# Optimization experiments

Hardware: AMD Instinct MI355X
Metric: run time of the kernel (lower is better)

Reference implementation:

```python
import jax, jax.numpy as jnp
import numpy as np

N_EMBD = 64
BLOCK = 8
HEADS = 4
HS = N_EMBD // HEADS  # 16
EPS = 1e-5


def layernorm(x, g, b):
    mu = jnp.mean(x, axis=-1, keepdims=True)
    var = jnp.var(x, axis=-1, keepdims=True)
    return (x - mu) * jax.lax.rsqrt(var + EPS) * g + b


def setup_inputs() -> dict:
    key = jax.random.key(0)
    ks = jax.random.split(key, 12)
    B = 65536
    s = 0.02
    return {
        "x": jax.random.normal(ks[0], (B, BLOCK, N_EMBD), dtype=jnp.float32),
        # per-head Q/K/V projections stacked: [H, C, hs]
        "Wq": jax.random.normal(ks[1], (HEADS, N_EMBD, HS), dtype=jnp.float32) * s,
        "Wk": jax.random.normal(ks[2], (HEADS, N_EMBD, HS), dtype=jnp.float32) * s,
        "Wv": jax.random.normal(ks[3], (HEADS, N_EMBD, HS), dtype=jnp.float32) * s,
        "Wp": jax.random.normal(ks[4], (N_EMBD, N_EMBD), dtype=jnp.float32) * s,
        "bp": jnp.zeros((N_EMBD,), dtype=jnp.float32),
        "W1": jax.random.normal(ks[5], (N_EMBD, 4 * N_EMBD), dtype=jnp.float32) * s,
        "b1": jnp.zeros((4 * N_EMBD,), dtype=jnp.float32),
        "W2": jax.random.normal(ks[6], (4 * N_EMBD, N_EMBD), dtype=jnp.float32) * s,
        "b2": jnp.zeros((N_EMBD,), dtype=jnp.float32),
        "g1": jnp.ones((N_EMBD,), dtype=jnp.float32),
        "beta1": jnp.zeros((N_EMBD,), dtype=jnp.float32),
        "g2": jnp.ones((N_EMBD,), dtype=jnp.float32),
        "beta2": jnp.zeros((N_EMBD,), dtype=jnp.float32),
    }


def reference(x, Wq, Wk, Wv, Wp, bp, W1, b1, W2, b2, g1, beta1, g2, beta2):
    B, T, C = x.shape
    # --- pre-LN self-attention ---
    h = layernorm(x, g1, beta1)
    q = jnp.einsum('btc,hcd->bhtd', h, Wq)
    k = jnp.einsum('btc,hcd->bhtd', h, Wk)
    v = jnp.einsum('btc,hcd->bhtd', h, Wv)
    # NOTE: original scales by n_embd**-0.5 (C of the input), not head_size
    wei = jnp.einsum('bhtd,bhsd->bhts', q, k) * (C ** -0.5)
    tril = jnp.tril(jnp.ones((T, T), dtype=bool))
    wei = jnp.where(tril, wei, -jnp.inf)
    wei = jax.nn.softmax(wei, axis=-1)  # dropout off (eval mode)
    attn = jnp.einsum('bhts,bhsd->bhtd', wei, v)
    attn = attn.transpose(0, 2, 1, 3).reshape(B, T, C)  # concat heads
    sa = attn @ Wp + bp
    x = x + sa
    # --- pre-LN MLP ---
    h2 = layernorm(x, g2, beta2)
    ff = jax.nn.relu(h2 @ W1 + b1) @ W2 + b2
    return x + ff
```

## Files before the change

### kernel.cpp

```cpp
#include <hip/hip_runtime.h>
#include <hip/hip_bf16.h>
#include <stdint.h>

typedef __attribute__((ext_vector_type(8))) short bf16x8;
typedef __attribute__((ext_vector_type(4))) float f32x4;


static __device__ __forceinline__ unsigned short f2bf(float f) {
    union { __hip_bfloat16 h; unsigned short u; } cv;
    cv.h = __float2bfloat16(f);
    return cv.u;
}
static __device__ __forceinline__ unsigned int f2bf2(float a, float b) {
    return (unsigned int)f2bf(a) | ((unsigned int)f2bf(b) << 16);
}
static __device__ __forceinline__ bf16x8 mk8(uint2 a, uint2 b) {
    union { uint4 u; bf16x8 v; } c;
    c.u = make_uint4(a.x, a.y, b.x, b.y);
    return c.v;
}
static __device__ __forceinline__ uint2 packbf(f32x4 a) {
    return make_uint2(f2bf2(a[0], a[1]), f2bf2(a[2], a[3]));
}
static __device__ __forceinline__ uint2 lnq(f32x4 x, float mu, float inv, f32x4 g, f32x4 b) {
    return make_uint2(f2bf2((x[0]-mu)*inv*g[0]+b[0], (x[1]-mu)*inv*g[1]+b[1]),
                      f2bf2((x[2]-mu)*inv*g[2]+b[2], (x[3]-mu)*inv*g[3]+b[3]));
}
static __device__ __forceinline__ uint2 relupack0(f32x4 a) {
    return make_uint2(f2bf2(fmaxf(a[0],0.f), fmaxf(a[1],0.f)),
                      f2bf2(fmaxf(a[2],0.f), fmaxf(a[3],0.f)));
}

#define MFMA(A,B,C) __builtin_amdgcn_mfma_f32_16x16x32_bf16((A),(B),(C),0,0,0)
#define SB() __builtin_amdgcn_sched_barrier(0)

static __device__ __forceinline__ uint2 attn_tail(f32x4 sa, uint2 vw, int fr, int fg) {
    const f32x4 zf = {0.f,0.f,0.f,0.f};
    const uint2 z2 = make_uint2(0u,0u);
    int tk0 = 4*fg, frq = fr & 7;
    bool v8 = ((fr ^ tk0) & 8) == 0;
    float p0 = (v8 && (((tk0+0)&7) <= frq)) ? __expf(sa[0]*0.125f) : 0.f;
    float p1 = (v8 && (((tk0+1)&7) <= frq)) ? __expf(sa[1]*0.125f) : 0.f;
    float p2 = (v8 && (((tk0+2)&7) <= frq)) ? __expf(sa[2]*0.125f) : 0.f;
    float p3 = (v8 && (((tk0+3)&7) <= frq)) ? __expf(sa[3]*0.125f) : 0.f;
    float rsum = p0 + p1 + p2 + p3;
    rsum += __shfl_xor(rsum, 16, 64);
    rsum += __shfl_xor(rsum, 32, 64);
    float pinv = __builtin_amdgcn_rcpf(rsum);
    uint2 pb = make_uint2(f2bf2(p0,p1), f2bf2(p2,p3));
    f32x4 oa = MFMA(mk8(vw, z2), mk8(pb, z2), zf);
    return make_uint2(f2bf2(oa[0]*pinv, oa[1]*pinv), f2bf2(oa[2]*pinv, oa[3]*pinv));
}

static __device__ __forceinline__ void attn_head2(
    bf16x8 wq0, bf16x8 wq1, bf16x8 wk0, bf16x8 wk1, bf16x8 wv0, bf16x8 wv1,
    bf16x8 hA0, bf16x8 hA1, bf16x8 hB0, bf16x8 hB1, int fr, int fg,
    uint2& oA, uint2& oB)
{
    const f32x4 zf = {0.f,0.f,0.f,0.f};
    const uint2 z2 = make_uint2(0u,0u);
    {
        f32x4 qa = MFMA(wq0, hA0, zf); qa = MFMA(wq1, hA1, qa);
        f32x4 ka = MFMA(wk0, hA0, zf); ka = MFMA(wk1, hA1, ka);
        f32x4 va = MFMA(hA0, wv0, zf); va = MFMA(hA1, wv1, va);
        uint2 qw = packbf(qa), kw = packbf(ka), vw = packbf(va);
        f32x4 sa = MFMA(mk8(kw, z2), mk8(qw, z2), zf);
        oA = attn_tail(sa, vw, fr, fg);
    }
    {
        f32x4 qa = MFMA(wq0, hB0, zf); qa = MFMA(wq1, hB1, qa);
        f32x4 ka = MFMA(wk0, hB0, zf); ka = MFMA(wk1, hB1, ka);
        f32x4 va = MFMA(hB0, wv0, zf); va = MFMA(hB1, wv1, va);
        uint2 qw = packbf(qa), kw = packbf(ka), vw = packbf(va);
        f32x4 sa = MFMA(mk8(kw, z2), mk8(qw, z2), zf);
        oB = attn_tail(sa, vw, fr, fg);
    }
}

__global__ __launch_bounds__(512, 1)
void fused_block(const float* __restrict__ xg,
                 const float* __restrict__ Wq, const float* __restrict__ Wk,
                 const float* __restrict__ Wv, const float* __restrict__ Wp,
                 const float* __restrict__ bp, const float* __restrict__ W1,
                 const float* __restrict__ b1, const float* __restrict__ W2,
                 const float* __restrict__ b2, const float* __restrict__ g1,
                 const float* __restrict__ be1, const float* __restrict__ g2,
                 const float* __restrict__ be2, float* __restrict__ out,
                 int nPairsTotal)
{
    __shared__ __align__(16) unsigned char LDS[100864];

    const int tid  = threadIdx.x;
    const int lane = tid & 63;
    const int wid  = tid >> 6;
    const int fr   = lane & 15;
    const int fg   = lane >> 4;

    {
        unsigned short* lw = (unsigned short*)LDS;
        #pragma unroll 1
        for (int e = tid; e < 49152; e += 512) {
            int j = e & 7, ln = (e >> 3) & 63, f = e >> 9;
            int fr_ = ln & 15, fg_ = ln >> 4;
            int u = j >> 2, r_ = j & 3;
            float src;
            if (f < 24) {
                int sel = f >> 3, hd = (f >> 1) & 3, m = f & 1;
                int c = 16*(2*m + u) + 4*fg_ + r_;
                const float* W = (sel == 0) ? Wq : ((sel == 1) ? Wk : Wv);
                src = W[hd*1024 + c*16 + fr_];
            } else if (f < 32) {
                int t = f - 24, nt = t >> 1, m = t & 1;
                int d = 16*(2*m + u) + 4*fg_ + r_;
                src = Wp[d*64 + 16*nt + fr_];
            } else if (f < 64) {
                int t = f - 32, tt = t >> 1, m = t & 1;
                int c = 16*(2*m + u) + 4*fg_ + r_;
                src = W1[c*256 + 16*tt + fr_];
            } else {
                int t = f - 64, nt = t >> 3, m = t & 7;
                int n1 = 16*(2*m + u) + 4*fg_ + r_;
                src = W2[n1*64 + 16*nt + fr_];
            }
            lw[e] = f2bf(src);
        }
    }
    #pragma unroll 1
    for (int t = tid; t < 640; t += 512) {
        float v;
        if      (t < 64)  v = g1[t];
        else if (t < 128) v = be1[t - 64];
        else if (t < 192) v = g2[t - 128];
        else if (t < 256) v = be2[t - 192];
        else if (t < 320) v = bp[t - 256];
        else if (t < 384) v = b2[t - 320];
        else              v = b1[t - 384];
        ((float*)(LDS + 98304))[t] = v;
    }
    __syncthreads();

    const float* PG = (const float*)(LDS + 98304);
    #define WFL(F) (*(const bf16x8*)(LDS + ((F) << 10) + (lane << 4)))
    #define PG4(I) (*(const f32x4*)(PG + (I) + 4*fg))

    const int pipe = blockIdx.x * 8 + wid;
    const f32x4 zf = {0.f, 0.f, 0.f, 0.f};
    const int xoff = fr*64 + 4*fg;
    const int nP2 = nPairsTotal >> 1;

    #pragma unroll 1
    for (int gp2 = pipe; gp2 < nP2; gp2 += 2048) {
        const float* xb = xg + (size_t)gp2 * 2048;
        float*      obp = out + (size_t)gp2 * 2048;

        f32x4 xA0 = *(const f32x4*)(xb + xoff);
        f32x4 xA1 = *(const f32x4*)(xb + xoff + 16);
        f32x4 xA2 = *(const f32x4*)(xb + xoff + 32);
        f32x4 xA3 = *(const f32x4*)(xb + xoff + 48);
        f32x4 xB0 = *(const f32x4*)(xb + 1024 + xoff);
        f32x4 xB1 = *(const f32x4*)(xb + 1024 + xoff + 16);
        f32x4 xB2 = *(const f32x4*)(xb + 1024 + xoff + 32);
        f32x4 xB3 = *(const f32x4*)(xb + 1024 + xoff + 48);
        SB();

        #define ACC4(S,SS,V) { S += V[0]+V[1]+V[2]+V[3]; \
                               SS += V[0]*V[0]+V[1]*V[1]+V[2]*V[2]+V[3]*V[3]; }

        bf16x8 hA0, hA1, hB0, hB1;
        {
            float sA=0.f, qA=0.f, sB=0.f, qB=0.f;
            ACC4(sA,qA,xA0); ACC4(sA,qA,xA1); ACC4(sA,qA,xA2); ACC4(sA,qA,xA3);
            ACC4(sB,qB,xB0); ACC4(sB,qB,xB1); ACC4(sB,qB,xB2); ACC4(sB,qB,xB3);
            sA += __shfl_xor(sA,16,64); qA += __shfl_xor(qA,16,64);
            sA += __shfl_xor(sA,32,64); qA += __shfl_xor(qA,32,64);
            sB += __shfl_xor(sB,16,64); qB += __shfl_xor(qB,16,64);
            sB += __shfl_xor(sB,32,64); qB += __shfl_xor(qB,32,64);
            float muA = sA*0.015625f, invA = rsqrtf(qA*0.015625f - muA*muA + 1e-5f);
            float muB = sB*0.015625f, invB = rsqrtf(qB*0.015625f - muB*muB + 1e-5f);
            hA0 = mk8(lnq(xA0,muA,invA,PG4(0),  PG4(64)),
                      lnq(xA1,muA,invA,PG4(16), PG4(80)));
            hA1 = mk8(lnq(xA2,muA,invA,PG4(32), PG4(96)),
                      lnq(xA3,muA,invA,PG4(48), PG4(112)));
            hB0 = mk8(lnq(xB0,muB,invB,PG4(0),  PG4(64)),
                      lnq(xB1,muB,invB,PG4(16), PG4(80)));
            hB1 = mk8(lnq(xB2,muB,invB,PG4(32), PG4(96)),
                      lnq(xB3,muB,invB,PG4(48), PG4(112)));
        }
        SB();

        uint2 oA0,oA1,oA2,oA3, oB0,oB1,oB2,oB3;
        attn_head2(WFL(0), WFL(1), WFL(8),  WFL(9),  WFL(16), WFL(17),
                   hA0,hA1, hB0,hB1, fr, fg, oA0, oB0);
        SB();
        attn_head2(WFL(2), WFL(3), WFL(10), WFL(11), WFL(18), WFL(19),
                   hA0,hA1, hB0,hB1, fr, fg, oA1, oB1);
        SB();
        attn_head2(WFL(4), WFL(5), WFL(12), WFL(13), WFL(20), WFL(21),
                   hA0,hA1, hB0,hB1, fr, fg, oA2, oB2);
        SB();
        attn_head2(WFL(6), WFL(7), WFL(14), WFL(15), WFL(22), WFL(23),
                   hA0,hA1, hB0,hB1, fr, fg, oA3, oB3);
        SB();

        {
            bf16x8 olo = mk8(oA0,oA1), ohi = mk8(oA2,oA3);
            bf16x8 plo = mk8(oB0,oB1), phi = mk8(oB2,oB3);
            #define PROJ(NT, XA, XB) { \
                f32x4 bv = PG4(256 + 16*(NT)); \
                f32x4 ca, cb; \
                ca[0]=XA[0]+bv[0]; ca[1]=XA[1]+bv[1]; ca[2]=XA[2]+bv[2]; ca[3]=XA[3]+bv[3]; \
                cb[0]=XB[0]+bv[0]; cb[1]=XB[1]+bv[1]; cb[2]=XB[2]+bv[2]; cb[3]=XB[3]+bv[3]; \
                bf16x8 wp0 = WFL(24+(NT)*2+0), wp1 = WFL(24+(NT)*2+1); \
                f32x4 pa = MFMA(wp0, olo, ca); pa = MFMA(wp1, ohi, pa); \
                f32x4 pb = MFMA(wp0, plo, cb); pb = MFMA(wp1, phi, pb); \
                XA = pa; XB = pb; }
            PROJ(0, xA0, xB0); PROJ(1, xA1, xB1); PROJ(2, xA2, xB2); PROJ(3, xA3, xB3);
            #undef PROJ
        }
        SB();

        bf16x8 cA0, cA1, cB0, cB1;
        f32x4 fA0, fA1, fA2, fA3, fB0, fB1, fB2, fB3;
        {
            float sA=0.f, qA=0.f, sB=0.f, qB=0.f;
            ACC4(sA,qA,xA0); ACC4(sA,qA,xA1); ACC4(sA,qA,xA2); ACC4(sA,qA,xA3);
            ACC4(sB,qB,xB0); ACC4(sB,qB,xB1); ACC4(sB,qB,xB2); ACC4(sB,qB,xB3);
            sA += __shfl_xor(sA,16,64); qA += __shfl_xor(qA,16,64);
            sA += __shfl_xor(sA,32,64); qA += __shfl_xor(qA,32,64);
            sB += __shfl_xor(sB,16,64); qB += __shfl_xor(qB,16,64);
            sB += __shfl_xor(sB,32,64); qB += __shfl_xor(qB,32,64);
            float muA = sA*0.015625f, invA = rsqrtf(qA*0.015625f - muA*muA + 1e-5f);
            float muB = sB*0.015625f, invB = rsqrtf(qB*0.015625f - muB*muB + 1e-5f);
            cA0 = mk8(lnq(xA0,muA,invA,PG4(128), PG4(192)),
                      lnq(xA1,muA,invA,PG4(144), PG4(208)));
            cA1 = mk8(lnq(xA2,muA,invA,PG4(160), PG4(224)),
                      lnq(xA3,muA,invA,PG4(176), PG4(240)));
            cB0 = mk8(lnq(xB0,muB,invB,PG4(128), PG4(192)),
                      lnq(xB1,muB,invB,PG4(144), PG4(208)));
            cB1 = mk8(lnq(xB2,muB,invB,PG4(160), PG4(224)),
                      lnq(xB3,muB,invB,PG4(176), PG4(240)));
            #define FINIT(NT, FA, FB, XA, XB) { \
                f32x4 bv = PG4(320 + 16*(NT)); \
                FA[0]=XA[0]+bv[0]; FA[1]=XA[1]+bv[1]; FA[2]=XA[2]+bv[2]; FA[3]=XA[3]+bv[3]; \
                FB[0]=XB[0]+bv[0]; FB[1]=XB[1]+bv[1]; FB[2]=XB[2]+bv[2]; FB[3]=XB[3]+bv[3]; }
            FINIT(0, fA0, fB0, xA0, xB0); FINIT(1, fA1, fB1, xA1, xB1);
            FINIT(2, fA2, fB2, xA2, xB2); FINIT(3, fA3, fB3, xA3, xB3);
            #undef FINIT
        }
        SB();

        #pragma unroll 1
        for (int m2 = 0; m2 < 8; ++m2) {
            int t0 = 2*m2, t1 = 2*m2 + 1;
            bf16x8 w10 = WFL(32+t0*2+0), w11 = WFL(32+t0*2+1);
            f32x4 bi0 = PG4(384 + 16*t0);
            f32x4 aA = MFMA(w10, cA0, bi0); aA = MFMA(w11, cA1, aA);
            f32x4 aB = MFMA(w10, cB0, bi0); aB = MFMA(w11, cB1, aB);
            uint2 frA0 = relupack0(aA), frB0 = relupack0(aB);
            bf16x8 w12 = WFL(32+t1*2+0), w13 = WFL(32+t1*2+1);
            f32x4 bi1 = PG4(384 + 16*t1);
            f32x4 cAa = MFMA(w12, cA0, bi1); cAa = MFMA(w13, cA1, cAa);
            f32x4 cBa = MFMA(w12, cB0, bi1); cBa = MFMA(w13, cB1, cBa);
            uint2 frA1 = relupack0(cAa), frB1 = relupack0(cBa);
            bf16x8 ffrA = mk8(frA0, frA1), ffrB = mk8(frB0, frB1);
            bf16x8 w20 = WFL(64 + 0*8 + m2);
            fA0 = MFMA(w20, ffrA, fA0); fB0 = MFMA(w20, ffrB, fB0);
            bf16x8 w21 = WFL(64 + 1*8 + m2);
            fA1 = MFMA(w21, ffrA, fA1); fB1 = MFMA(w21, ffrB, fB1);
            bf16x8 w22 = WFL(64 + 2*8 + m2);
            fA2 = MFMA(w22, ffrA, fA2); fB2 = MFMA(w22, ffrB, fB2);
            bf16x8 w23 = WFL(64 + 3*8 + m2);
            fA3 = MFMA(w23, ffrA, fA3); fB3 = MFMA(w23, ffrB, fB3);
            SB();
        }

        *(f32x4*)(obp + xoff)             = fA0;
        *(f32x4*)(obp + xoff + 16)        = fA1;
        *(f32x4*)(obp + xoff + 32)        = fA2;
        *(f32x4*)(obp + xoff + 48)        = fA3;
        *(f32x4*)(obp + 1024 + xoff)      = fB0;
        *(f32x4*)(obp + 1024 + xoff + 16) = fB1;
        *(f32x4*)(obp + 1024 + xoff + 32) = fB2;
        *(f32x4*)(obp + 1024 + xoff + 48) = fB3;
        #undef ACC4
    }
    #undef WFL
    #undef PG4
}

extern "C" void kernel_launch(void* const* d_in, const int* in_sizes, int n_in,
                              void* d_out, int out_size, void* d_ws, size_t ws_size,
                              hipStream_t stream) {
    const float* x   = (const float*)d_in[0];
    const float* Wq  = (const float*)d_in[1];
    const float* Wk  = (const float*)d_in[2];
    const float* Wv  = (const float*)d_in[3];
    const float* Wp  = (const float*)d_in[4];
    const float* bp  = (const float*)d_in[5];
    const float* W1  = (const float*)d_in[6];
    const float* b1  = (const float*)d_in[7];
    const float* W2  = (const float*)d_in[8];
    const float* b2  = (const float*)d_in[9];
    const float* g1  = (const float*)d_in[10];
    const float* be1 = (const float*)d_in[11];
    const float* g2  = (const float*)d_in[12];
    const float* be2 = (const float*)d_in[13];
    int nPairs = in_sizes[0] / 1024;
    fused_block<<<dim3(256), dim3(512), 0, stream>>>(
        x, Wq, Wk, Wv, Wp, bp, W1, b1, W2, b2, g1, be1, g2, be2,
        (float*)d_out, nPairs);
}
```

Baseline: 117.8 us.

## Pre-pack bf16 weights in a separate kernel and copy them into LDS

```diff
diff --git a/kernel.cpp b/kernel.cpp
--- a/kernel.cpp
+++ b/kernel.cpp
@@ -77,15 +77,59 @@
     }
 }
 
+__global__ __launch_bounds__(512)
+void pack_weights(const float* __restrict__ Wq, const float* __restrict__ Wk,
+                  const float* __restrict__ Wv, const float* __restrict__ Wp,
+                  const float* __restrict__ W1, const float* __restrict__ W2,
+                  const float* __restrict__ bp, const float* __restrict__ b1,
+                  const float* __restrict__ b2, const float* __restrict__ g1,
+                  const float* __restrict__ be1, const float* __restrict__ g2,
+                  const float* __restrict__ be2, unsigned short* __restrict__ gw)
+{
+    int e = blockIdx.x * 512 + threadIdx.x;
+    if (e < 49152) {
+        int j = e & 7, ln = (e >> 3) & 63, f = e >> 9;
+        int fr_ = ln & 15, fg_ = ln >> 4;
+        int u = j >> 2, r_ = j & 3;
+        float src;
+        if (f < 24) {
+            int sel = f >> 3, hd = (f >> 1) & 3, m = f & 1;
+            int c = 16*(2*m + u) + 4*fg_ + r_;
+            const float* W = (sel == 0) ? Wq : ((sel == 1) ? Wk : Wv);
+            src = W[hd*1024 + c*16 + fr_];
+        } else if (f < 32) {
+            int t = f - 24, nt = t >> 1, m = t & 1;
+            int d = 16*(2*m + u) + 4*fg_ + r_;
+            src = Wp[d*64 + 16*nt + fr_];
+        } else if (f < 64) {
+            int t = f - 32, tt = t >> 1, m = t & 1;
+            int c = 16*(2*m + u) + 4*fg_ + r_;
+            src = W1[c*256 + 16*tt + fr_];
+        } else {
+            int t = f - 64, nt = t >> 3, m = t & 7;
+            int n1 = 16*(2*m + u) + 4*fg_ + r_;
+            src = W2[n1*64 + 16*nt + fr_];
+        }
+        gw[e] = f2bf(src);
+    } else {
+        int t = e - 49152;
+        if (t < 640) {
+            float v;
+            if      (t < 64)  v = g1[t];
+            else if (t < 128) v = be1[t - 64];
+            else if (t < 192) v = g2[t - 128];
+            else if (t < 256) v = be2[t - 192];
+            else if (t < 320) v = bp[t - 256];
+            else if (t < 384) v = b2[t - 320];
+            else              v = b1[t - 384];
+            ((float*)(gw + 49152))[t] = v;
+        }
+    }
+}
+
 __global__ __launch_bounds__(512, 1)
-void fused_block(const float* __restrict__ xg,
-                 const float* __restrict__ Wq, const float* __restrict__ Wk,
-                 const float* __restrict__ Wv, const float* __restrict__ Wp,
-                 const float* __restrict__ bp, const float* __restrict__ W1,
-                 const float* __restrict__ b1, const float* __restrict__ W2,
-                 const float* __restrict__ b2, const float* __restrict__ g1,
-                 const float* __restrict__ be1, const float* __restrict__ g2,
-                 const float* __restrict__ be2, float* __restrict__ out,
+void fused_block(const unsigned short* __restrict__ gw,
+                 const float* __restrict__ xg, float* __restrict__ out,
                  int nPairsTotal)
 {
     __shared__ __align__(16) unsigned char LDS[100864];
@@ -97,45 +141,12 @@
     const int fg   = lane >> 4;
 
     {
-        unsigned short* lw = (unsigned short*)LDS;
-        #pragma unroll 1
-        for (int e = tid; e < 49152; e += 512) {
-            int j = e & 7, ln = (e >> 3) & 63, f = e >> 9;
-            int fr_ = ln & 15, fg_ = ln >> 4;
-            int u = j >> 2, r_ = j & 3;
-            float src;
-            if (f < 24) {
-                int sel = f >> 3, hd = (f >> 1) & 3, m = f & 1;
-                int c = 16*(2*m + u) + 4*fg_ + r_;
-                const float* W = (sel == 0) ? Wq : ((sel == 1) ? Wk : Wv);
-                src = W[hd*1024 + c*16 + fr_];
-            } else if (f < 32) {
-                int t = f - 24, nt = t >> 1, m = t & 1;
-                int d = 16*(2*m + u) + 4*fg_ + r_;
-                src = Wp[d*64 + 16*nt + fr_];
-            } else if (f < 64) {
-                int t = f - 32, tt = t >> 1, m = t & 1;
-                int c = 16*(2*m + u) + 4*fg_ + r_;
-                src = W1[c*256 + 16*tt + fr_];
-            } else {
-                int t = f - 64, nt = t >> 3, m = t & 7;
-                int n1 = 16*(2*m + u) + 4*fg_ + r_;
-                src = W2[n1*64 + 16*nt + fr_];
-            }
-            lw[e] = f2bf(src);
-        }
-    }
-    #pragma unroll 1
-    for (int t = tid; t < 640; t += 512) {
-        float v;
-        if      (t < 64)  v = g1[t];
-        else if (t < 128) v = be1[t - 64];
-        else if (t < 192) v = g2[t - 128];
-        else if (t < 256) v = be2[t - 192];
-        else if (t < 320) v = bp[t - 256];
-        else if (t < 384) v = b2[t - 320];
-        else              v = b1[t - 384];
-        ((float*)(LDS + 98304))[t] = v;
+        const uint4* src = (const uint4*)gw;
+        uint4* dst = (uint4*)LDS;
+        #pragma unroll
+        for (int k = 0; k < 12; ++k)
+            dst[tid + 512*k] = src[tid + 512*k];
+        if (tid < 160) dst[tid + 6144] = src[tid + 6144];
     }
     __syncthreads();
 
@@ -191,13 +202,11 @@
         uint2 oA0,oA1,oA2,oA3, oB0,oB1,oB2,oB3;
         attn_head2(WFL(0), WFL(1), WFL(8),  WFL(9),  WFL(16), WFL(17),
                    hA0,hA1, hB0,hB1, fr, fg, oA0, oB0);
-        SB();
         attn_head2(WFL(2), WFL(3), WFL(10), WFL(11), WFL(18), WFL(19),
                    hA0,hA1, hB0,hB1, fr, fg, oA1, oB1);
         SB();
         attn_head2(WFL(4), WFL(5), WFL(12), WFL(13), WFL(20), WFL(21),
                    hA0,hA1, hB0,hB1, fr, fg, oA2, oB2);
-        SB();
         attn_head2(WFL(6), WFL(7), WFL(14), WFL(15), WFL(22), WFL(23),
                    hA0,hA1, hB0,hB1, fr, fg, oA3, oB3);
         SB();
@@ -271,7 +280,6 @@
             fA2 = MFMA(w22, ffrA, fA2); fB2 = MFMA(w22, ffrB, fB2);
             bf16x8 w23 = WFL(64 + 3*8 + m2);
             fA3 = MFMA(w23, ffrA, fA3); fB3 = MFMA(w23, ffrB, fB3);
-            SB();
         }
 
         *(f32x4*)(obp + xoff)             = fA0;
@@ -305,8 +313,12 @@
     const float* be1 = (const float*)d_in[11];
     const float* g2  = (const float*)d_in[12];
     const float* be2 = (const float*)d_in[13];
+    unsigned short* gw = (unsigned short*)d_ws;
+
+    pack_weights<<<dim3(98), dim3(512), 0, stream>>>(
+        Wq, Wk, Wv, Wp, W1, W2, bp, b1, b2, g1, be1, g2, be2, gw);
+
     int nPairs = in_sizes[0] / 1024;
     fused_block<<<dim3(256), dim3(512), 0, stream>>>(
-        x, Wq, Wk, Wv, Wp, bp, W1, b1, W2, b2, g1, be1, g2, be2,
-        (float*)d_out, nPairs);
-}
+        gw, x, (float*)d_out, nPairs);
+}
```

After: 97.08 us. 1.21x faster.
